# Kernel tuning notes

Measured on AMD Instinct MI355X. Metric: run time of the kernel, lower is better.

The kernel has to match this reference:

```python
import jax, jax.numpy as jnp
import numpy as np

N, D, E, R, EJ = 100000, 128, 600000, 200, 300000


def setup_inputs() -> dict:
    key = jax.random.key(0)
    ks = jax.random.split(key, 14)
    s = 1.0 / np.sqrt(D)
    return {
        "emb": jax.random.normal(ks[0], (N, D), jnp.float32),
        "change": jax.random.normal(ks[1], (N, D), jnp.float32),
        "W1": jax.random.normal(ks[2], (D, D), jnp.float32) * s,
        "Wloop1": jax.random.normal(ks[3], (D, D), jnp.float32) * s,
        "rel_emb1": jax.random.normal(ks[4], (R, D), jnp.float32),
        "W2": jax.random.normal(ks[5], (D, D), jnp.float32) * s,
        "Wloop2": jax.random.normal(ks[6], (D, D), jnp.float32) * s,
        "rel_emb2": jax.random.normal(ks[7], (R, D), jnp.float32),
        "res": jnp.array([0.1], jnp.float32),
        "jump_weight": jnp.array([1.0], jnp.float32),
        "edge_w_jump": jax.random.uniform(ks[8], (EJ,), jnp.float32),
        "edge_index": jax.random.randint(ks[9], (2, E), 0, N, jnp.int32),
        "edge_type": jax.random.randint(ks[10], (E,), 0, R, jnp.int32),
        "edge_id_jump": jax.random.randint(ks[11], (2, EJ), 0, N, jnp.int32),
    }


def _mgcn_conv(x, W, Wloop, rel_emb, edge_index, edge_type, num_e):
    # Relational (CompGCN-style mult composition) conv: gather-compose-scatter.
    src, dst = edge_index[0], edge_index[1]
    msg = x[src] * rel_emb[edge_type]                      # [E, D]
    agg = jax.ops.segment_sum(msg, dst, num_segments=num_e)
    deg = jax.ops.segment_sum(jnp.ones(src.shape, x.dtype), dst, num_segments=num_e)
    agg = agg / jnp.maximum(deg, 1.0)[:, None]
    return jnp.tanh(agg @ W + x @ Wloop)


def reference(emb, change, W1, Wloop1, rel_emb1, W2, Wloop2, rel_emb2, res,
              jump_weight, edge_w_jump, edge_index, edge_type, edge_id_jump):
    num_e = emb.shape[0]
    jump_emb = emb
    # residual-scaled two-layer relational GCN (dropout = identity in eval)
    h = emb + res[0] * _mgcn_conv(emb, W1, Wloop1, rel_emb1, edge_index, edge_type, num_e)
    h = h + res[0] * _mgcn_conv(h, W2, Wloop2, rel_emb2, edge_index, edge_type, num_e)
    # jump diffusion: weighted scatter over jump edge list
    jsrc, jdst = edge_id_jump[0], edge_id_jump[1]
    jump_res = jax.ops.segment_sum(edge_w_jump[:, None] * jump_emb[jsrc], jdst,
                                   num_segments=num_e)
    dchange = h + jump_weight[0] * jump_res
    return (change, dchange)
```

## Files before the change

kernel.cpp:

```cpp
#include <hip/hip_runtime.h>
#include <math.h>

#define D 128

typedef __attribute__((ext_vector_type(8))) short short8v;
typedef __attribute__((ext_vector_type(4))) float f32x4;

__device__ inline short f2bf(float f) {
    unsigned u = __float_as_uint(f);
    u += 0x7FFF + ((u >> 16) & 1);
    return (short)(u >> 16);
}
__device__ inline float bf2f(unsigned short s) {
    return __uint_as_float(((unsigned)s) << 16);
}
__device__ inline float fast_tanh(float x) {
    float a = fabsf(x);
    float e = __expf(-2.0f * a);
    float t = (1.0f - e) / (1.0f + e);
    return copysignf(t, x);
}

__global__ void hist_both(const int* __restrict__ dst_e,
                          const int* __restrict__ dst_j,
                          int* __restrict__ cnt, int E, int EJ, int N) {
    int i = blockIdx.x * blockDim.x + threadIdx.x;
    if (i < E) atomicAdd(&cnt[dst_e[i]], 1);
    else if (i < E + EJ) atomicAdd(&cnt[N + dst_j[i - E]], 1);
}

__global__ void scan1(const int* __restrict__ cnt, int* __restrict__ offs,
                      int* __restrict__ bsum, int M) {
    __shared__ int sh[256];
    int t = threadIdx.x;
    int base = blockIdx.x * 1024 + t * 4;
    int v0 = 0, v1 = 0, v2 = 0, v3 = 0;
    if (base + 0 < M) v0 = cnt[base + 0];
    if (base + 1 < M) v1 = cnt[base + 1];
    if (base + 2 < M) v2 = cnt[base + 2];
    if (base + 3 < M) v3 = cnt[base + 3];
    int tsum = v0 + v1 + v2 + v3;
    sh[t] = tsum;
    __syncthreads();
    for (int off = 1; off < 256; off <<= 1) {
        int x = (t >= off) ? sh[t - off] : 0;
        __syncthreads();
        sh[t] += x;
        __syncthreads();
    }
    int excl = sh[t] - tsum;
    if (base + 0 < M) offs[base + 0] = excl;
    excl += v0;
    if (base + 1 < M) offs[base + 1] = excl;
    excl += v1;
    if (base + 2 < M) offs[base + 2] = excl;
    excl += v2;
    if (base + 3 < M) offs[base + 3] = excl;
    if (t == 255) bsum[blockIdx.x] = sh[255];
}

__global__ void scan2(int* __restrict__ bsum, int NB) {
    __shared__ int sh[256];
    int t = threadIdx.x;
    int v = (t < NB) ? bsum[t] : 0;
    sh[t] = v;
    __syncthreads();
    for (int off = 1; off < 256; off <<= 1) {
        int x = (t >= off) ? sh[t - off] : 0;
        __syncthreads();
        sh[t] += x;
        __syncthreads();
    }
    if (t < NB) bsum[t] = sh[t] - v;
}

__global__ void scan3(int* __restrict__ offs, const int* __restrict__ bsum,
                      int* __restrict__ cur, int M) {
    int i = blockIdx.x * blockDim.x + threadIdx.x;
    if (i < M) {
        int o = offs[i] + bsum[i >> 10];
        offs[i] = o;
        cur[i] = o;
    }
}

__global__ void fill_both(const int* __restrict__ src_e,
                          const int* __restrict__ dst_e,
                          const int* __restrict__ et,
                          const int* __restrict__ src_j,
                          const int* __restrict__ dst_j,
                          const float* __restrict__ ew,
                          int* __restrict__ cur, int2* __restrict__ pairs,
                          int E, int EJ, int N) {
    int i = blockIdx.x * blockDim.x + threadIdx.x;
    if (i < E) {
        int p = atomicAdd(&cur[dst_e[i]], 1);
        pairs[p] = make_int2(src_e[i], et[i]);
    } else if (i < E + EJ) {
        int e = i - E;
        int p = atomicAdd(&cur[N + dst_j[e]], 1);
        pairs[p] = make_int2(src_j[e], __float_as_int(ew[e]));
    }
}

__global__ void pack_w(const float* __restrict__ W1, const float* __restrict__ Wl1,
                       const float* __restrict__ W2, const float* __restrict__ Wl2,
                       short* __restrict__ B1, short* __restrict__ B2) {
    int lane = threadIdx.x;
    int tile = blockIdx.x & 63;
    const float* W  = (blockIdx.x < 64) ? W1 : W2;
    const float* Wl = (blockIdx.x < 64) ? Wl1 : Wl2;
    short* Bpk      = (blockIdx.x < 64) ? B1 : B2;
    int tn = tile >> 3, tk = tile & 7;
    int n = tn * 16 + (lane & 15);
    int k0 = tk * 32 + (lane >> 4) * 8;
    short* o = Bpk + ((size_t)tile * 64 + lane) * 8;
#pragma unroll
    for (int j = 0; j < 8; j++) {
        int k = k0 + j;
        float f = (k < D) ? W[(size_t)k * D + n] : Wl[(size_t)(k - D) * D + n];
        o[j] = f2bf(f);
    }
}

__global__ void cvt_rel(const float* __restrict__ r1, const float* __restrict__ r2,
                        short* __restrict__ o1, short* __restrict__ o2, int RD) {
    int i = blockIdx.x * blockDim.x + threadIdx.x;
    int half = RD >> 2;
    if (i < 2 * half) {
        const float* src = (i < half) ? r1 : r2;
        short* dst = (i < half) ? o1 : o2;
        int j = (i < half) ? i : i - half;
        float4 v = *(const float4*)(src + (size_t)j * 4);
        short4 o;
        o.x = f2bf(v.x); o.y = f2bf(v.y); o.z = f2bf(v.z); o.w = f2bf(v.w);
        *(short4*)(dst + (size_t)j * 4) = o;
    } else {
        int extra = i - 2 * half;
        if (extra < 64) {
            short* dst = (extra < 32) ? o1 : o2;
            int j = extra & 31;
            short4 z; z.x = 0; z.y = 0; z.z = 0; z.w = 0;
            *(short4*)(dst + (size_t)RD + j * 4) = z;
        }
    }
}

__global__ void cvt_emb_copy(const float* __restrict__ emb,
                             const float* __restrict__ change,
                             short* __restrict__ Abf,
                             float* __restrict__ out, int N) {
    int i = blockIdx.x * blockDim.x + threadIdx.x;
    int row = i >> 5;
    int c4 = (i & 31) * 4;
    if (row >= N) return;
    float4 v = *(const float4*)(emb + (size_t)row * D + c4);
    short4 o;
    o.x = f2bf(v.x); o.y = f2bf(v.y); o.z = f2bf(v.z); o.w = f2bf(v.w);
    *(short4*)(Abf + (size_t)row * 256 + 128 + c4) = o;
    float4 ch = *(const float4*)(change + (size_t)row * D + c4);
    *(float4*)(out + (size_t)row * D + c4) = ch;
}

__global__ void gather_conv(short* __restrict__ Abf,
                            const short* __restrict__ relb,
                            const int* __restrict__ offs,
                            const int* __restrict__ cnt,
                            const int2* __restrict__ pairs, int N, int RZ) {
    int node = blockIdx.x * 4 + (threadIdx.x >> 6);
    if (node >= N) return;
    int lane = threadIdx.x & 63;
    int h = lane >> 4;
    int c = (lane & 15) * 8;
    int beg = offs[node], num = cnt[node];
    float acc[8];
#pragma unroll
    for (int j = 0; j < 8; j++) acc[j] = 0.f;
    if (num > 0) {
        int ia = h, ib = h + 4;
        int ea = (ia < num) ? ia : (num - 1);
        int2 pa = pairs[beg + ea];
        int ra = (ia < num) ? pa.y : RZ;
        short8v xa = *(const short8v*)(Abf + (size_t)pa.x * 256 + 128 + c);
        short8v va = *(const short8v*)(relb + (size_t)ra * D + c);
        if (num > 4) {
            int eb = (ib < num) ? ib : (num - 1);
            int2 pb = pairs[beg + eb];
            int rb = (ib < num) ? pb.y : RZ;
            short8v xb = *(const short8v*)(Abf + (size_t)pb.x * 256 + 128 + c);
            short8v vb = *(const short8v*)(relb + (size_t)rb * D + c);
#pragma unroll
            for (int j = 0; j < 8; j++)
                acc[j] += bf2f((unsigned short)xa[j]) * bf2f((unsigned short)va[j]);
#pragma unroll
            for (int j = 0; j < 8; j++)
                acc[j] += bf2f((unsigned short)xb[j]) * bf2f((unsigned short)vb[j]);
        } else {
#pragma unroll
            for (int j = 0; j < 8; j++)
                acc[j] += bf2f((unsigned short)xa[j]) * bf2f((unsigned short)va[j]);
        }
        for (int i = 8; i < num; i += 4) {
            int ei = i + h;
            int e2 = (ei < num) ? ei : (num - 1);
            int2 pe = pairs[beg + e2];
            int rr = (ei < num) ? pe.y : RZ;
            short8v xv = *(const short8v*)(Abf + (size_t)pe.x * 256 + 128 + c);
            short8v rv = *(const short8v*)(relb + (size_t)rr * D + c);
#pragma unroll
            for (int j = 0; j < 8; j++)
                acc[j] += bf2f((unsigned short)xv[j]) * bf2f((unsigned short)rv[j]);
        }
#pragma unroll
        for (int j = 0; j < 8; j++) {
            acc[j] += __shfl_xor(acc[j], 16);
            acc[j] += __shfl_xor(acc[j], 32);
        }
    }
    if (h == 0) {
        float dinv = 1.0f / fmaxf((float)num, 1.0f);
        short8v o;
#pragma unroll
        for (int j = 0; j < 8; j++) o[j] = f2bf(acc[j] * dinv);
        *(short8v*)(Abf + (size_t)node * 256 + c) = o;
    }
}

__global__ void gather_phase2(short* __restrict__ Abf2,
                              const short* __restrict__ Abf1,
                              const short* __restrict__ relb,
                              const float* __restrict__ jwp,
                              const int* __restrict__ offs,
                              const int* __restrict__ cnt,
                              const int2* __restrict__ pairs,
                              float* __restrict__ dch, int N, int RZ) {
    int g = blockIdx.x * 4 + (threadIdx.x >> 6);
    int lane = threadIdx.x & 63;
    int h = lane >> 4;
    int c = (lane & 15) * 8;
    if (g < N) {
        int beg = offs[g], num = cnt[g];
        float acc[8];
#pragma unroll
        for (int j = 0; j < 8; j++) acc[j] = 0.f;
        if (num > 0) {
            int ia = h, ib = h + 4;
            int ea = (ia < num) ? ia : (num - 1);
            int2 pa = pairs[beg + ea];
            int ra = (ia < num) ? pa.y : RZ;
            short8v xa = *(const short8v*)(Abf2 + (size_t)pa.x * 256 + 128 + c);
            short8v va = *(const short8v*)(relb + (size_t)ra * D + c);
            if (num > 4) {
                int eb = (ib < num) ? ib : (num - 1);
                int2 pb = pairs[beg + eb];
                int rb = (ib < num) ? pb.y : RZ;
                short8v xb = *(const short8v*)(Abf2 + (size_t)pb.x * 256 + 128 + c);
                short8v vb = *(const short8v*)(relb + (size_t)rb * D + c);
#pragma unroll
                for (int j = 0; j < 8; j++)
                    acc[j] += bf2f((unsigned short)xa[j]) * bf2f((unsigned short)va[j]);
#pragma unroll
                for (int j = 0; j < 8; j++)
                    acc[j] += bf2f((unsigned short)xb[j]) * bf2f((unsigned short)vb[j]);
            } else {
#pragma unroll
                for (int j = 0; j < 8; j++)
                    acc[j] += bf2f((unsigned short)xa[j]) * bf2f((unsigned short)va[j]);
            }
            for (int i = 8; i < num; i += 4) {
                int ei = i + h;
                int e2 = (ei < num) ? ei : (num - 1);
                int2 pe = pairs[beg + e2];
                int rr = (ei < num) ? pe.y : RZ;
                short8v xv = *(const short8v*)(Abf2 + (size_t)pe.x * 256 + 128 + c);
                short8v rv = *(const short8v*)(relb + (size_t)rr * D + c);
#pragma unroll
                for (int j = 0; j < 8; j++)
                    acc[j] += bf2f((unsigned short)xv[j]) * bf2f((unsigned short)rv[j]);
            }
#pragma unroll
            for (int j = 0; j < 8; j++) {
                acc[j] += __shfl_xor(acc[j], 16);
                acc[j] += __shfl_xor(acc[j], 32);
            }
        }
        if (h == 0) {
            float dinv = 1.0f / fmaxf((float)num, 1.0f);
            short8v o;
#pragma unroll
            for (int j = 0; j < 8; j++) o[j] = f2bf(acc[j] * dinv);
            *(short8v*)(Abf2 + (size_t)g * 256 + c) = o;
        }
    } else if (g < 2 * N) {
        int node = g - N;
        int beg = offs[N + node], num = cnt[N + node];
        float acc[8];
#pragma unroll
        for (int j = 0; j < 8; j++) acc[j] = 0.f;
        if (num > 0) {
            int ia = h, ib = h + 4;
            int ea = (ia < num) ? ia : (num - 1);
            int2 pa = pairs[beg + ea];
            float wa = (ia < num) ? __int_as_float(pa.y) : 0.f;
            short8v xa = *(const short8v*)(Abf1 + (size_t)pa.x * 256 + 128 + c);
            if (num > 4) {
                int eb = (ib < num) ? ib : (num - 1);
                int2 pb = pairs[beg + eb];
                float wb = (ib < num) ? __int_as_float(pb.y) : 0.f;
                short8v xb = *(const short8v*)(Abf1 + (size_t)pb.x * 256 + 128 + c);
#pragma unroll
                for (int j = 0; j < 8; j++)
                    acc[j] += wa * bf2f((unsigned short)xa[j]);
#pragma unroll
                for (int j = 0; j < 8; j++)
                    acc[j] += wb * bf2f((unsigned short)xb[j]);
            } else {
#pragma unroll
                for (int j = 0; j < 8; j++)
                    acc[j] += wa * bf2f((unsigned short)xa[j]);
            }
            for (int i = 8; i < num; i += 4) {
                int ei = i + h;
                int e2 = (ei < num) ? ei : (num - 1);
                int2 pe = pairs[beg + e2];
                float wgt = (ei < num) ? __int_as_float(pe.y) : 0.f;
                short8v xv = *(const short8v*)(Abf1 + (size_t)pe.x * 256 + 128 + c);
#pragma unroll
                for (int j = 0; j < 8; j++)
                    acc[j] += wgt * bf2f((unsigned short)xv[j]);
            }
#pragma unroll
            for (int j = 0; j < 8; j++) {
                acc[j] += __shfl_xor(acc[j], 16);
                acc[j] += __shfl_xor(acc[j], 32);
            }
        }
        if (h == 0) {
            float jw = jwp[0];
            float* drow = dch + (size_t)node * D + c;
            *(float4*)(drow + 0) = make_float4(jw * acc[0], jw * acc[1],
                                               jw * acc[2], jw * acc[3]);
            *(float4*)(drow + 4) = make_float4(jw * acc[4], jw * acc[5],
                                               jw * acc[6], jw * acc[7]);
        }
    }
}

__launch_bounds__(256)
__global__ void mfma_gemm(const short* __restrict__ Abf,
                          const short* __restrict__ Bpk,
                          const float* __restrict__ resp,
                          short* __restrict__ outb,
                          const float* __restrict__ addin,
                          float* __restrict__ outf,
                          int N) {
    int w = threadIdx.x >> 6;
    int lane = threadIdx.x & 63;
    int rb = (w & 1) * 32;
    int cb = (w >> 1) * 64;
    int row0 = blockIdx.x * 64;
    int m = lane & 15, quad = lane >> 4;

    f32x4 acc[2][4];
#pragma unroll
    for (int rt = 0; rt < 2; rt++)
#pragma unroll
        for (int ct = 0; ct < 4; ct++) acc[rt][ct] = (f32x4)(0.f);

    const short* arow0 = Abf + (size_t)(row0 + rb + m) * 256 + quad * 8;
    const short* arow1 = arow0 + 16 * 256;
    const short* bbase = Bpk + (((size_t)(cb >> 4)) * 8 * 64 + lane) * 8;

#pragma unroll
    for (int kt = 0; kt < 8; kt++) {
        short8v a0 = *(const short8v*)(arow0 + kt * 32);
        short8v a1 = *(const short8v*)(arow1 + kt * 32);
        short8v b[4];
#pragma unroll
        for (int ct = 0; ct < 4; ct++)
            b[ct] = *(const short8v*)(bbase + ((size_t)(ct * 8 + kt)) * 64 * 8);
#pragma unroll
        for (int ct = 0; ct < 4; ct++) {
            acc[0][ct] = __builtin_amdgcn_mfma_f32_16x16x32_bf16(a0, b[ct],
                                                                 acc[0][ct], 0, 0, 0);
            acc[1][ct] = __builtin_amdgcn_mfma_f32_16x16x32_bf16(a1, b[ct],
                                                                 acc[1][ct], 0, 0, 0);
        }
    }

    float res = resp[0];
#pragma unroll
    for (int rt = 0; rt < 2; rt++) {
#pragma unroll
        for (int ct = 0; ct < 4; ct++) {
            int colg = cb + ct * 16 + m;
#pragma unroll
            for (int r = 0; r < 4; r++) {
                int rowg = row0 + rb + rt * 16 + quad * 4 + r;
                if (rowg >= N) continue;
                float xr = bf2f((unsigned short)Abf[(size_t)rowg * 256 + 128 + colg]);
                float o = xr + res * fast_tanh(acc[rt][ct][r]);
                if (outb != nullptr) {
                    outb[(size_t)rowg * 256 + 128 + colg] = f2bf(o);
                } else {
                    size_t idx = (size_t)rowg * D + colg;
                    outf[idx] = o + addin[idx];
                }
            }
        }
    }
}

extern "C" void kernel_launch(void* const* d_in, const int* in_sizes, int n_in,
                              void* d_out, int out_size, void* d_ws, size_t ws_size,
                              hipStream_t stream) {
    const float* emb    = (const float*)d_in[0];
    const float* change = (const float*)d_in[1];
    const float* W1     = (const float*)d_in[2];
    const float* Wl1    = (const float*)d_in[3];
    const float* rel1   = (const float*)d_in[4];
    const float* W2     = (const float*)d_in[5];
    const float* Wl2    = (const float*)d_in[6];
    const float* rel2   = (const float*)d_in[7];
    const float* res    = (const float*)d_in[8];
    const float* jw     = (const float*)d_in[9];
    const float* ewj    = (const float*)d_in[10];
    const int*   eidx   = (const int*)d_in[11];
    const int*   etype  = (const int*)d_in[12];
    const int*   ejmp   = (const int*)d_in[13];

    const int ND = in_sizes[0];
    const int N  = ND / D;
    const int E  = in_sizes[12];
    const int EJ = in_sizes[10];
    const int RD = in_sizes[4];
    const int R  = RD / D;
    const int NP = ((N + 63) / 64) * 64;
    const int M  = 2 * N;

    float* out = (float*)d_out;
    float* dch = out + (size_t)ND;

    char* w = (char*)d_ws;
    short* Abf1  = (short*)w;                  w += (size_t)NP * 256 * 2;
    short* Abf2  = (short*)w;                  w += (size_t)NP * 256 * 2;
    short* Bpk1  = (short*)w;                  w += (size_t)64 * 64 * 8 * 2;
    short* Bpk2  = (short*)w;                  w += (size_t)64 * 64 * 8 * 2;
    short* relb1 = (short*)w;                  w += (size_t)(RD + D) * 2;
    short* relb2 = (short*)w;                  w += (size_t)(RD + D) * 2;
    int* cnt     = (int*)w;                    w += (size_t)M * 4;
    int* offs    = (int*)w;                    w += (size_t)M * 4;
    int* cur     = (int*)w;                    w += (size_t)M * 4;
    int* bsum    = (int*)w;                    w += 256 * 4;
    int2* pairs  = (int2*)w;                   w += (size_t)(E + EJ) * 8;

    const int T = 256;
    const int NB2 = (M + 1023) / 1024;
    const int EB  = (E + EJ + T - 1) / T;

    hipMemsetAsync(cnt, 0, (size_t)M * sizeof(int), stream);

    hist_both<<<EB, T, 0, stream>>>(eidx + E, ejmp + EJ, cnt, E, EJ, N);
    scan1<<<NB2, 256, 0, stream>>>(cnt, offs, bsum, M);
    scan2<<<1, 256, 0, stream>>>(bsum, NB2);
    scan3<<<(M + T - 1) / T, T, 0, stream>>>(offs, bsum, cur, M);
    fill_both<<<EB, T, 0, stream>>>(eidx, eidx + E, etype, ejmp, ejmp + EJ, ewj,
                                    cur, pairs, E, EJ, N);

    pack_w<<<128, 64, 0, stream>>>(W1, Wl1, W2, Wl2, Bpk1, Bpk2);
    cvt_rel<<<(RD / 2 + 64 + T - 1) / T, T, 0, stream>>>(rel1, rel2, relb1, relb2, RD);

    cvt_emb_copy<<<(N * 32 + T - 1) / T, T, 0, stream>>>(emb, change, Abf1, out, N);

    int gatherB  = (N + 3) / 4;
    int gather2B = (M + 3) / 4;
    int gemmB    = NP / 64;

    gather_conv<<<gatherB, 256, 0, stream>>>(Abf1, relb1, offs, cnt, pairs, N, R);
    mfma_gemm<<<gemmB, 256, 0, stream>>>(Abf1, Bpk1, res, Abf2, nullptr, nullptr, N);

    gather_phase2<<<gather2B, 256, 0, stream>>>(Abf2, Abf1, relb2, jw, offs, cnt,
                                                pairs, dch, N, R);

    mfma_gemm<<<gemmB, 256, 0, stream>>>(Abf2, Bpk2, res, nullptr, dch, dch, N);
}
```

Baseline: 519.2 us.

## Switch to fp16 storage and MFMA, gather node features as 8-bit e5m2

Moves every intermediate buffer and the GEMMs from bf16 to fp16 and adds a separate 8-bit e5m2-style copy of the node features, which the relational gathers read in place of the 16-bit rows. The gather kernels now accumulate in packed half2 FMAs instead of fp32 scalar FMAs. The goal is to halve the random-gather bytes for the edge messages and to cut ALU work in the gathers. The cost is extra byte stores in the GEMM epilogue and the conversion kernel, plus much lower precision: 2-bit-mantissa inputs and fp16 accumulation over many edges, which may exceed the accuracy tolerance or overflow.

```diff
diff --git a/kernel.cpp b/kernel.cpp
--- a/kernel.cpp
+++ b/kernel.cpp
@@ -5,20 +5,49 @@
 
 typedef __attribute__((ext_vector_type(8))) short short8v;
 typedef __attribute__((ext_vector_type(4))) float f32x4;
-
-__device__ inline short f2bf(float f) {
-    unsigned u = __float_as_uint(f);
-    u += 0x7FFF + ((u >> 16) & 1);
-    return (short)(u >> 16);
-}
-__device__ inline float bf2f(unsigned short s) {
-    return __uint_as_float(((unsigned)s) << 16);
-}
+typedef _Float16 half2n __attribute__((ext_vector_type(2)));
+typedef _Float16 half8v __attribute__((ext_vector_type(8)));
+
+__device__ inline short f2h(float f) {
+    _Float16 h = (_Float16)f;
+    return __builtin_bit_cast(short, h);
+}
+__device__ inline float h2f(short s) {
+    return (float)__builtin_bit_cast(_Float16, s);
+}
+__device__ inline unsigned char h2e5(short hs) {
+    unsigned u = (unsigned short)hs;
+    u = u + 0x7Fu + ((u >> 8) & 1u);
+    return (unsigned char)(u >> 8);
+}
+__device__ inline half2n u2h2(unsigned u) { return __builtin_bit_cast(half2n, u); }
+__device__ inline unsigned h22u(half2n h) { return __builtin_bit_cast(unsigned, h); }
+
 __device__ inline float fast_tanh(float x) {
     float a = fabsf(x);
     float e = __expf(-2.0f * a);
     float t = (1.0f - e) / (1.0f + e);
     return copysignf(t, x);
+}
+
+__device__ inline void e5fma(uint2 xw, uint4 rw,
+                             half2n& a0, half2n& a1, half2n& a2, half2n& a3) {
+    a0 += u2h2(xw.x & 0xFF00FF00u) * u2h2(rw.x);
+    a1 += u2h2((xw.x << 8) & 0xFF00FF00u) * u2h2(rw.y);
+    a2 += u2h2(xw.y & 0xFF00FF00u) * u2h2(rw.z);
+    a3 += u2h2((xw.y << 8) & 0xFF00FF00u) * u2h2(rw.w);
+}
+__device__ inline void h16fma(uint4 xw, half2n w2,
+                              half2n& a0, half2n& a1, half2n& a2, half2n& a3) {
+    a0 += u2h2(xw.x) * w2;
+    a1 += u2h2(xw.y) * w2;
+    a2 += u2h2(xw.z) * w2;
+    a3 += u2h2(xw.w) * w2;
+}
+__device__ inline half2n red2(half2n a) {
+    a += u2h2((unsigned)__shfl_xor(__builtin_bit_cast(int, a), 16));
+    a += u2h2((unsigned)__shfl_xor(__builtin_bit_cast(int, a), 32));
+    return a;
 }
 
 __global__ void hist_both(const int* __restrict__ dst_e,
@@ -119,7 +148,7 @@
     for (int j = 0; j < 8; j++) {
         int k = k0 + j;
         float f = (k < D) ? W[(size_t)k * D + n] : Wl[(size_t)(k - D) * D + n];
-        o[j] = f2bf(f);
+        o[j] = f2h(f);
     }
 }
 
@@ -133,7 +162,7 @@
         int j = (i < half) ? i : i - half;
         float4 v = *(const float4*)(src + (size_t)j * 4);
         short4 o;
-        o.x = f2bf(v.x); o.y = f2bf(v.y); o.z = f2bf(v.z); o.w = f2bf(v.w);
+        o.x = f2h(v.x); o.y = f2h(v.y); o.z = f2h(v.z); o.w = f2h(v.w);
         *(short4*)(dst + (size_t)j * 4) = o;
     } else {
         int extra = i - 2 * half;
@@ -149,6 +178,7 @@
 __global__ void cvt_emb_copy(const float* __restrict__ emb,
                              const float* __restrict__ change,
                              short* __restrict__ Abf,
+                             unsigned char* __restrict__ X8,
                              float* __restrict__ out, int N) {
     int i = blockIdx.x * blockDim.x + threadIdx.x;
     int row = i >> 5;
@@ -156,14 +186,18 @@
     if (row >= N) return;
     float4 v = *(const float4*)(emb + (size_t)row * D + c4);
     short4 o;
-    o.x = f2bf(v.x); o.y = f2bf(v.y); o.z = f2bf(v.z); o.w = f2bf(v.w);
+    o.x = f2h(v.x); o.y = f2h(v.y); o.z = f2h(v.z); o.w = f2h(v.w);
     *(short4*)(Abf + (size_t)row * 256 + 128 + c4) = o;
+    unsigned u = (unsigned)h2e5(o.z) | ((unsigned)h2e5(o.x) << 8) |
+                 ((unsigned)h2e5(o.w) << 16) | ((unsigned)h2e5(o.y) << 24);
+    *(unsigned*)(X8 + (size_t)row * 128 + c4) = u;
     float4 ch = *(const float4*)(change + (size_t)row * D + c4);
     *(float4*)(out + (size_t)row * D + c4) = ch;
 }
 
-__global__ void gather_conv(short* __restrict__ Abf,
+__global__ void gather_conv(const unsigned char* __restrict__ X8,
                             const short* __restrict__ relb,
+                            short* __restrict__ Abf,
                             const int* __restrict__ offs,
                             const int* __restrict__ cnt,
                             const int2* __restrict__ pairs, int N, int RZ) {
@@ -173,60 +207,48 @@
     int h = lane >> 4;
     int c = (lane & 15) * 8;
     int beg = offs[node], num = cnt[node];
-    float acc[8];
-#pragma unroll
-    for (int j = 0; j < 8; j++) acc[j] = 0.f;
+    half2n a0 = u2h2(0u), a1 = u2h2(0u), a2 = u2h2(0u), a3 = u2h2(0u);
     if (num > 0) {
         int ia = h, ib = h + 4;
         int ea = (ia < num) ? ia : (num - 1);
         int2 pa = pairs[beg + ea];
         int ra = (ia < num) ? pa.y : RZ;
-        short8v xa = *(const short8v*)(Abf + (size_t)pa.x * 256 + 128 + c);
-        short8v va = *(const short8v*)(relb + (size_t)ra * D + c);
+        uint2 xa = *(const uint2*)(X8 + (size_t)pa.x * 128 + c);
+        uint4 va = *(const uint4*)(relb + (size_t)ra * D + c);
         if (num > 4) {
             int eb = (ib < num) ? ib : (num - 1);
             int2 pb = pairs[beg + eb];
             int rb = (ib < num) ? pb.y : RZ;
-            short8v xb = *(const short8v*)(Abf + (size_t)pb.x * 256 + 128 + c);
-            short8v vb = *(const short8v*)(relb + (size_t)rb * D + c);
-#pragma unroll
-            for (int j = 0; j < 8; j++)
-                acc[j] += bf2f((unsigned short)xa[j]) * bf2f((unsigned short)va[j]);
-#pragma unroll
-            for (int j = 0; j < 8; j++)
-                acc[j] += bf2f((unsigned short)xb[j]) * bf2f((unsigned short)vb[j]);
+            uint2 xb = *(const uint2*)(X8 + (size_t)pb.x * 128 + c);
+            uint4 vb = *(const uint4*)(relb + (size_t)rb * D + c);
+            e5fma(xa, va, a0, a1, a2, a3);
+            e5fma(xb, vb, a0, a1, a2, a3);
         } else {
-#pragma unroll
-            for (int j = 0; j < 8; j++)
-                acc[j] += bf2f((unsigned short)xa[j]) * bf2f((unsigned short)va[j]);
+            e5fma(xa, va, a0, a1, a2, a3);
         }
         for (int i = 8; i < num; i += 4) {
             int ei = i + h;
             int e2 = (ei < num) ? ei : (num - 1);
             int2 pe = pairs[beg + e2];
             int rr = (ei < num) ? pe.y : RZ;
-            short8v xv = *(const short8v*)(Abf + (size_t)pe.x * 256 + 128 + c);
-            short8v rv = *(const short8v*)(relb + (size_t)rr * D + c);
-#pragma unroll
-            for (int j = 0; j < 8; j++)
-                acc[j] += bf2f((unsigned short)xv[j]) * bf2f((unsigned short)rv[j]);
-        }
-#pragma unroll
-        for (int j = 0; j < 8; j++) {
-            acc[j] += __shfl_xor(acc[j], 16);
-            acc[j] += __shfl_xor(acc[j], 32);
-        }
+            uint2 xv = *(const uint2*)(X8 + (size_t)pe.x * 128 + c);
+            uint4 rv = *(const uint4*)(relb + (size_t)rr * D + c);
+            e5fma(xv, rv, a0, a1, a2, a3);
+        }
+        a0 = red2(a0); a1 = red2(a1); a2 = red2(a2); a3 = red2(a3);
     }
     if (h == 0) {
         float dinv = 1.0f / fmaxf((float)num, 1.0f);
-        short8v o;
-#pragma unroll
-        for (int j = 0; j < 8; j++) o[j] = f2bf(acc[j] * dinv);
-        *(short8v*)(Abf + (size_t)node * 256 + c) = o;
+        _Float16 dh = (_Float16)dinv;
+        half2n d2 = {dh, dh};
+        a0 *= d2; a1 *= d2; a2 *= d2; a3 *= d2;
+        uint4 st; st.x = h22u(a0); st.y = h22u(a1); st.z = h22u(a2); st.w = h22u(a3);
+        *(uint4*)(Abf + (size_t)node * 256 + c) = st;
     }
 }
 
 __global__ void gather_phase2(short* __restrict__ Abf2,
+                              const unsigned char* __restrict__ X82,
                               const short* __restrict__ Abf1,
                               const short* __restrict__ relb,
                               const float* __restrict__ jwp,
@@ -240,108 +262,87 @@
     int c = (lane & 15) * 8;
     if (g < N) {
         int beg = offs[g], num = cnt[g];
-        float acc[8];
-#pragma unroll
-        for (int j = 0; j < 8; j++) acc[j] = 0.f;
+        half2n a0 = u2h2(0u), a1 = u2h2(0u), a2 = u2h2(0u), a3 = u2h2(0u);
         if (num > 0) {
             int ia = h, ib = h + 4;
             int ea = (ia < num) ? ia : (num - 1);
             int2 pa = pairs[beg + ea];
             int ra = (ia < num) ? pa.y : RZ;
-            short8v xa = *(const short8v*)(Abf2 + (size_t)pa.x * 256 + 128 + c);
-            short8v va = *(const short8v*)(relb + (size_t)ra * D + c);
+            uint2 xa = *(const uint2*)(X82 + (size_t)pa.x * 128 + c);
+            uint4 va = *(const uint4*)(relb + (size_t)ra * D + c);
             if (num > 4) {
                 int eb = (ib < num) ? ib : (num - 1);
                 int2 pb = pairs[beg + eb];
                 int rb = (ib < num) ? pb.y : RZ;
-                short8v xb = *(const short8v*)(Abf2 + (size_t)pb.x * 256 + 128 + c);
-                short8v vb = *(const short8v*)(relb + (size_t)rb * D + c);
-#pragma unroll
-                for (int j = 0; j < 8; j++)
-                    acc[j] += bf2f((unsigned short)xa[j]) * bf2f((unsigned short)va[j]);
-#pragma unroll
-                for (int j = 0; j < 8; j++)
-                    acc[j] += bf2f((unsigned short)xb[j]) * bf2f((unsigned short)vb[j]);
+                uint2 xb = *(const uint2*)(X82 + (size_t)pb.x * 128 + c);
+                uint4 vb = *(const uint4*)(relb + (size_t)rb * D + c);
+                e5fma(xa, va, a0, a1, a2, a3);
+                e5fma(xb, vb, a0, a1, a2, a3);
             } else {
-#pragma unroll
-                for (int j = 0; j < 8; j++)
-                    acc[j] += bf2f((unsigned short)xa[j]) * bf2f((unsigned short)va[j]);
+                e5fma(xa, va, a0, a1, a2, a3);
             }
             for (int i = 8; i < num; i += 4) {
                 int ei = i + h;
                 int e2 = (ei < num) ? ei : (num - 1);
                 int2 pe = pairs[beg + e2];
                 int rr = (ei < num) ? pe.y : RZ;
-                short8v xv = *(const short8v*)(Abf2 + (size_t)pe.x * 256 + 128 + c);
-                short8v rv = *(const short8v*)(relb + (size_t)rr * D + c);
-#pragma unroll
-                for (int j = 0; j < 8; j++)
-                    acc[j] += bf2f((unsigned short)xv[j]) * bf2f((unsigned short)rv[j]);
+                uint2 xv = *(const uint2*)(X82 + (size_t)pe.x * 128 + c);
+                uint4 rv = *(const uint4*)(relb + (size_t)rr * D + c);
+                e5fma(xv, rv, a0, a1, a2, a3);
             }
-#pragma unroll
-            for (int j = 0; j < 8; j++) {
-                acc[j] += __shfl_xor(acc[j], 16);
-                acc[j] += __shfl_xor(acc[j], 32);
-            }
+            a0 = red2(a0); a1 = red2(a1); a2 = red2(a2); a3 = red2(a3);
         }
         if (h == 0) {
             float dinv = 1.0f / fmaxf((float)num, 1.0f);
-            short8v o;
-#pragma unroll
-            for (int j = 0; j < 8; j++) o[j] = f2bf(acc[j] * dinv);
-            *(short8v*)(Abf2 + (size_t)g * 256 + c) = o;
+            _Float16 dh = (_Float16)dinv;
+            half2n d2 = {dh, dh};
+            a0 *= d2; a1 *= d2; a2 *= d2; a3 *= d2;
+            uint4 st; st.x = h22u(a0); st.y = h22u(a1); st.z = h22u(a2); st.w = h22u(a3);
+            *(uint4*)(Abf2 + (size_t)g * 256 + c) = st;
         }
     } else if (g < 2 * N) {
         int node = g - N;
         int beg = offs[N + node], num = cnt[N + node];
-        float acc[8];
-#pragma unroll
-        for (int j = 0; j < 8; j++) acc[j] = 0.f;
+        half2n a0 = u2h2(0u), a1 = u2h2(0u), a2 = u2h2(0u), a3 = u2h2(0u);
         if (num > 0) {
             int ia = h, ib = h + 4;
             int ea = (ia < num) ? ia : (num - 1);
             int2 pa = pairs[beg + ea];
             float wa = (ia < num) ? __int_as_float(pa.y) : 0.f;
-            short8v xa = *(const short8v*)(Abf1 + (size_t)pa.x * 256 + 128 + c);
+            _Float16 wha = (_Float16)wa;
+            half2n w2a = {wha, wha};
+            uint4 xa = *(const uint4*)(Abf1 + (size_t)pa.x * 256 + 128 + c);
             if (num > 4) {
                 int eb = (ib < num) ? ib : (num - 1);
                 int2 pb = pairs[beg + eb];
                 float wb = (ib < num) ? __int_as_float(pb.y) : 0.f;
-                short8v xb = *(const short8v*)(Abf1 + (size_t)pb.x * 256 + 128 + c);
-#pragma unroll
-                for (int j = 0; j < 8; j++)
-                    acc[j] += wa * bf2f((unsigned short)xa[j]);
-#pragma unroll
-                for (int j = 0; j < 8; j++)
-                    acc[j] += wb * bf2f((unsigned short)xb[j]);
+                _Float16 whb = (_Float16)wb;
+                half2n w2b = {whb, whb};
+                uint4 xb = *(const uint4*)(Abf1 + (size_t)pb.x * 256 + 128 + c);
+                h16fma(xa, w2a, a0, a1, a2, a3);
+                h16fma(xb, w2b, a0, a1, a2, a3);
             } else {
-#pragma unroll
-                for (int j = 0; j < 8; j++)
-                    acc[j] += wa * bf2f((unsigned short)xa[j]);
+                h16fma(xa, w2a, a0, a1, a2, a3);
             }
             for (int i = 8; i < num; i += 4) {
                 int ei = i + h;
                 int e2 = (ei < num) ? ei : (num - 1);
                 int2 pe = pairs[beg + e2];
                 float wgt = (ei < num) ? __int_as_float(pe.y) : 0.f;
-                short8v xv = *(const short8v*)(Abf1 + (size_t)pe.x * 256 + 128 + c);
-#pragma unroll
-                for (int j = 0; j < 8; j++)
-                    acc[j] += wgt * bf2f((unsigned short)xv[j]);
+                _Float16 wh = (_Float16)wgt;
+                half2n w2 = {wh, wh};
+                uint4 xv = *(const uint4*)(Abf1 + (size_t)pe.x * 256 + 128 + c);
+                h16fma(xv, w2, a0, a1, a2, a3);
             }
-#pragma unroll
-            for (int j = 0; j < 8; j++) {
-                acc[j] += __shfl_xor(acc[j], 16);
-                acc[j] += __shfl_xor(acc[j], 32);
-            }
+            a0 = red2(a0); a1 = red2(a1); a2 = red2(a2); a3 = red2(a3);
         }
         if (h == 0) {
             float jw = jwp[0];
             float* drow = dch + (size_t)node * D + c;
-            *(float4*)(drow + 0) = make_float4(jw * acc[0], jw * acc[1],
-                                               jw * acc[2], jw * acc[3]);
-            *(float4*)(drow + 4) = make_float4(jw * acc[4], jw * acc[5],
-                                               jw * acc[6], jw * acc[7]);
+            *(float4*)(drow + 0) = make_float4(jw * (float)a0.x, jw * (float)a0.y,
+                                               jw * (float)a1.x, jw * (float)a1.y);
+            *(float4*)(drow + 4) = make_float4(jw * (float)a2.x, jw * (float)a2.y,
+                                               jw * (float)a3.x, jw * (float)a3.y);
         }
     }
 }
@@ -351,6 +352,7 @@
                           const short* __restrict__ Bpk,
                           const float* __restrict__ resp,
                           short* __restrict__ outb,
+                          unsigned char* __restrict__ x8out,
                           const float* __restrict__ addin,
                           float* __restrict__ outf,
                           int N) {
@@ -373,18 +375,18 @@
 
 #pragma unroll
     for (int kt = 0; kt < 8; kt++) {
-        short8v a0 = *(const short8v*)(arow0 + kt * 32);
-        short8v a1 = *(const short8v*)(arow1 + kt * 32);
-        short8v b[4];
+        half8v a0 = *(const half8v*)(arow0 + kt * 32);
+        half8v a1 = *(const half8v*)(arow1 + kt * 32);
+        half8v b[4];
 #pragma unroll
         for (int ct = 0; ct < 4; ct++)
-            b[ct] = *(const short8v*)(bbase + ((size_t)(ct * 8 + kt)) * 64 * 8);
+            b[ct] = *(const half8v*)(bbase + ((size_t)(ct * 8 + kt)) * 64 * 8);
 #pragma unroll
         for (int ct = 0; ct < 4; ct++) {
-            acc[0][ct] = __builtin_amdgcn_mfma_f32_16x16x32_bf16(a0, b[ct],
-                                                                 acc[0][ct], 0, 0, 0);
-            acc[1][ct] = __builtin_amdgcn_mfma_f32_16x16x32_bf16(a1, b[ct],
-                                                                 acc[1][ct], 0, 0, 0);
+            acc[0][ct] = __builtin_amdgcn_mfma_f32_16x16x32_f16(a0, b[ct],
+                                                                acc[0][ct], 0, 0, 0);
+            acc[1][ct] = __builtin_amdgcn_mfma_f32_16x16x32_f16(a1, b[ct],
+                                                                acc[1][ct], 0, 0, 0);
         }
     }
 
@@ -398,10 +400,14 @@
             for (int r = 0; r < 4; r++) {
                 int rowg = row0 + rb + rt * 16 + quad * 4 + r;
                 if (rowg >= N) continue;
-                float xr = bf2f((unsigned short)Abf[(size_t)rowg * 256 + 128 + colg]);
+                float xr = h2f(Abf[(size_t)rowg * 256 + 128 + colg]);
                 float o = xr + res * fast_tanh(acc[rt][ct][r]);
                 if (outb != nullptr) {
-                    outb[(size_t)rowg * 256 + 128 + colg] = f2bf(o);
+                    short hx = f2h(o);
+                    outb[(size_t)rowg * 256 + 128 + colg] = hx;
+                    int d = colg & 3;
+                    int pos = 2 * (d & 1) + 1 - (d >> 1);
+                    x8out[(size_t)rowg * 128 + (colg & ~3) + pos] = h2e5(hx);
                 } else {
                     size_t idx = (size_t)rowg * D + colg;
                     outf[idx] = o + addin[idx];
@@ -448,6 +454,8 @@
     short* Bpk2  = (short*)w;                  w += (size_t)64 * 64 * 8 * 2;
     short* relb1 = (short*)w;                  w += (size_t)(RD + D) * 2;
     short* relb2 = (short*)w;                  w += (size_t)(RD + D) * 2;
+    unsigned char* X81 = (unsigned char*)w;    w += (size_t)NP * 128;
+    unsigned char* X82 = (unsigned char*)w;    w += (size_t)NP * 128;
     int* cnt     = (int*)w;                    w += (size_t)M * 4;
     int* offs    = (int*)w;                    w += (size_t)M * 4;
     int* cur     = (int*)w;                    w += (size_t)M * 4;
@@ -470,17 +478,17 @@
     pack_w<<<128, 64, 0, stream>>>(W1, Wl1, W2, Wl2, Bpk1, Bpk2);
     cvt_rel<<<(RD / 2 + 64 + T - 1) / T, T, 0, stream>>>(rel1, rel2, relb1, relb2, RD);
 
-    cvt_emb_copy<<<(N * 32 + T - 1) / T, T, 0, stream>>>(emb, change, Abf1, out, N);
+    cvt_emb_copy<<<(N * 32 + T - 1) / T, T, 0, stream>>>(emb, change, Abf1, X81, out, N);
 
     int gatherB  = (N + 3) / 4;
     int gather2B = (M + 3) / 4;
     int gemmB    = NP / 64;
 
-    gather_conv<<<gatherB, 256, 0, stream>>>(Abf1, relb1, offs, cnt, pairs, N, R);
-    mfma_gemm<<<gemmB, 256, 0, stream>>>(Abf1, Bpk1, res, Abf2, nullptr, nullptr, N);
-
-    gather_phase2<<<gather2B, 256, 0, stream>>>(Abf2, Abf1, relb2, jw, offs, cnt,
+    gather_conv<<<gatherB, 256, 0, stream>>>(X81, relb1, Abf1, offs, cnt, pairs, N, R);
+    mfma_gemm<<<gemmB, 256, 0, stream>>>(Abf1, Bpk1, res, Abf2, X82, nullptr, nullptr, N);
+
+    gather_phase2<<<gather2B, 256, 0, stream>>>(Abf2, X82, Abf1, relb2, jw, offs, cnt,
                                                 pairs, dch, N, R);
 
-    mfma_gemm<<<gemmB, 256, 0, stream>>>(Abf2, Bpk2, res, nullptr, dch, dch, N);
-}
+    mfma_gemm<<<gemmB, 256, 0, stream>>>(Abf2, Bpk2, res, nullptr, nullptr, dch, dch, N);
+}
```

After: 523.0 us. Within noise of the previous version (+0.7%).
